# Kernel optimization log

Measured on AMD Instinct MI355X. Metric: run time of the kernel, lower is better.

## Reference

```python
import jax, jax.numpy as jnp
import numpy as np

B, C, S, K, HEADS, P = 2, 64, 112, 7, 4, 3
DH = C // HEADS

def _na_idx(L, k):
    # NATTEN-style clamped windows: each query attends to k in-bounds neighbors
    i = np.arange(L)
    s = np.clip(i - k // 2, 0, L - k)
    nbr = s[:, None] + np.arange(k)[None, :]      # (L,k) absolute neighbor index
    rel = nbr - i[:, None] + (k - 1)              # (L,k) rel-pos-bias index in [0,2k-2]
    return jnp.asarray(nbr), jnp.asarray(rel)

def _ln(x, g, b, eps=1e-5):
    m = jnp.mean(x, -1, keepdims=True)
    v = jnp.mean(jnp.square(x - m), -1, keepdims=True)
    return (x - m) * jax.lax.rsqrt(v + eps) * g + b

def _conv(x, w, b):
    y = jax.lax.conv_general_dilated(x, w, (1, 1), [(P // 2, P // 2)] * 2,
                                     dimension_numbers=('NCHW', 'OIHW', 'NCHW'))
    return jnp.transpose(y + b[None, :, None, None], (0, 2, 3, 1))  # NHWC

def setup_inputs():
    key = jax.random.key(0)
    ks = jax.random.split(key, 24)
    r = lambda i, shape, s=0.02: jax.random.normal(ks[i], shape, jnp.float32) * s
    return {
        'xq': jax.random.normal(ks[0], (B, C, S, S), jnp.float32),
        'xkv': jax.random.normal(ks[1], (B, C, S, S), jnp.float32),
        'conv_w_s': r(2, (C, C, P, P)), 'conv_b_s': r(3, (C,), 0.01),
        'conv_w_l': r(4, (C, C, P, P)), 'conv_b_l': r(5, (C,), 0.01),
        'g_s': jnp.ones((C,), jnp.float32), 'b_s': jnp.zeros((C,), jnp.float32),
        'g_l': jnp.ones((C,), jnp.float32), 'b_l': jnp.zeros((C,), jnp.float32),
        'Wq': r(6, (C, C)), 'bq': r(7, (C,), 0.01),
        'Wk': r(8, (C, C)), 'bk': r(9, (C,), 0.01),
        'Wv': r(10, (C, C)), 'bv': r(11, (C,), 0.01),
        'Wo': r(12, (C, C)), 'bo': r(13, (C,), 0.01),
        'rpb': r(14, (HEADS, 2 * K - 1, 2 * K - 1)),
        'g_n': jnp.ones((C,), jnp.float32), 'b_n': jnp.zeros((C,), jnp.float32),
        'W1': r(15, (C, 2 * C)), 'b1': r(16, (2 * C,), 0.01),
        'W2': r(17, (2 * C, C)), 'b2': r(18, (C,), 0.01),
    }

def reference(xq, xkv, conv_w_s, conv_b_s, conv_w_l, conv_b_l, g_s, b_s, g_l, b_l,
              Wq, bq, Wk, bk, Wv, bv, Wo, bo, rpb, g_n, b_n, W1, b1, W2, b2):
    emb_q = _conv(xq, conv_w_s, conv_b_s)     # (B,H,W,C) overlap patch embed (q branch)
    emb_kv = _conv(xkv, conv_w_l, conv_b_l)   # (B,H,W,C)
    Hh, Ww = emb_q.shape[1], emb_q.shape[2]
    qn = _ln(emb_q, g_s, b_s)
    kvn = _ln(emb_kv, g_l, b_l)
    q = (qn @ Wq + bq).reshape(B, Hh, Ww, HEADS, DH)
    k = (kvn @ Wk + bk).reshape(B, Hh, Ww, HEADS, DH)
    v = (kvn @ Wv + bv).reshape(B, Hh, Ww, HEADS, DH)
    ni, ri = _na_idx(Hh, K)
    nj, rj = _na_idx(Ww, K)

    def gather(t):  # (B,H,W,h,d) -> (B,H,W,K*K,h,d) neighborhood windows
        t = t[:, ni]                                 # (B,H,K,W,h,d)
        t = t[:, :, :, nj]                           # (B,H,K,W,K,h,d)
        t = jnp.transpose(t, (0, 1, 3, 2, 4, 5, 6))  # (B,H,W,K,K,h,d)
        return t.reshape(B, Hh, Ww, K * K, HEADS, DH)

    kg, vg = gather(k), gather(v)
    logits = jnp.einsum('bijhd,bijnhd->bhijn', q, kg) * (DH ** -0.5)
    bias = rpb[:, ri]                                # (h,H,K,2K-1)
    bias = bias[:, :, :, rj]                         # (h,H,K,W,K)
    bias = jnp.transpose(bias, (0, 1, 3, 2, 4)).reshape(HEADS, Hh, Ww, K * K)
    attn = jax.nn.softmax(logits + bias[None], axis=-1)
    out = jnp.einsum('bhijn,bijnhd->bijhd', attn, vg).reshape(B, Hh, Ww, C)
    att = out @ Wo + bo + emb_kv                     # residual with kv embedding
    x = _ln(att, g_n, b_n)
    x = jax.nn.gelu(x @ W1 + b1, approximate=False) @ W2 + b2 + att
    return jnp.transpose(x, (0, 3, 1, 2))            # (B,C,H,W)
```

## Files before the change

### kernel.cpp

```cpp
#include <hip/hip_runtime.h>
#include <math.h>

#define SS 112
#define HW (SS*SS)
#define NPIX (2*HW)

typedef __bf16 v8bf __attribute__((ext_vector_type(8)));
typedef short  v8s  __attribute__((ext_vector_type(8)));
typedef float  v4f  __attribute__((ext_vector_type(4)));

__device__ __forceinline__ unsigned short f2bf(float f){
  unsigned u = __builtin_bit_cast(unsigned, f);
  u = (u + 0x7fffu + ((u >> 16) & 1u)) >> 16;
  return (unsigned short)u;
}
__device__ __forceinline__ unsigned cvt_pk_bf16(float lo, float hi){
  unsigned r;
  asm("v_cvt_pk_bf16_f32 %0, %1, %2" : "=v"(r) : "v"(lo), "v"(hi));
  return r;
}
__device__ __forceinline__ v8bf zero8(){
  v8s z = {0,0,0,0,0,0,0,0};
  return __builtin_bit_cast(v8bf, z);
}
__device__ __forceinline__ float gelu_fast(float x){
  float u = fmaf(0.044715f*x, x, 1.0f);
  float z = fminf(2.3021178f * x * u, 80.0f);
  float s = exp2f(z);
  return x * s * __builtin_amdgcn_rcpf(s + 1.0f);
}

struct Params {
  const float *xq, *xkv, *cws, *cwl, *Wq, *Wk, *Wv, *Wo, *W1, *W2, *rpb;
  const float *cbs, *g_s, *b_s, *cbl, *g_l, *b_l;
  const float *bq, *bk, *bv, *bo, *gn, *bn, *b1, *b2;
  unsigned short *WBs, *WBl, *WBq, *WBk, *WBv, *WBo, *WB1, *WB2;
  float *rpb2g;
  unsigned short *xTq, *xTkv, *qb, *kb, *vT;
  float *emb, *outp;
};

__device__ __forceinline__ void pack_wconv(const float* __restrict__ w,
                                           unsigned short* __restrict__ WB, int idx){
  int lane = idx & 63, tslot = (idx >> 6) & 3, kk = idx >> 8;
  int tap = kk >> 1;
  int ic0 = ((kk & 1) << 5) + ((lane >> 4) << 3);
  int oc  = tslot*16 + (lane & 15);
  union { unsigned short u[8]; uint4 q; } pk;
  #pragma unroll
  for (int i = 0; i < 8; ++i) pk.u[i] = f2bf(w[(oc*64 + ic0 + i)*9 + tap]);
  ((uint4*)WB)[idx] = pk.q;
}
__device__ __forceinline__ void pack_wlin(const float* __restrict__ W,
                                          unsigned short* __restrict__ WB,
                                          int N, int idx){
  int lane = idx & 63;
  int tmp = idx >> 6;
  int tiles = N >> 4;
  int tslot = tmp % tiles;
  int kk = tmp / tiles;
  int k0 = kk*32 + ((lane >> 4) << 3);
  int oc = tslot*16 + (lane & 15);
  union { unsigned short u[8]; uint4 q; } pk;
  #pragma unroll
  for (int i = 0; i < 8; ++i) pk.u[i] = f2bf(W[(size_t)(k0 + i)*N + oc]);
  ((uint4*)WB)[idx] = pk.q;
}

__global__ __launch_bounds__(256) void k_prep_s(Params P)
{
  __shared__ float tile[64][68];
  const int u = blockIdx.x, tid = threadIdx.x;
  if (u >= 784){
    const int pu = u - 784;
    if      (pu < 18) pack_wconv(P.cws, P.WBs, pu*256 + tid);
    else if (pu < 36) pack_wconv(P.cwl, P.WBl, (pu-18)*256 + tid);
    else if (pu < 38) pack_wlin(P.Wq, P.WBq, 64,  (pu-36)*256 + tid);
    else if (pu < 40) pack_wlin(P.Wk, P.WBk, 64,  (pu-38)*256 + tid);
    else if (pu < 42) pack_wlin(P.Wv, P.WBv, 64,  (pu-40)*256 + tid);
    else if (pu < 44) pack_wlin(P.Wo, P.WBo, 64,  (pu-42)*256 + tid);
    else if (pu < 48) pack_wlin(P.W1, P.WB1, 128, (pu-44)*256 + tid);
    else if (pu < 52) pack_wlin(P.W2, P.WB2, 64,  (pu-48)*256 + tid);
    else {
      int idx = (pu-52)*256 + tid;
      if (idx < 4*169) P.rpb2g[idx] = P.rpb[idx] * 1.4426950408889634f;
    }
    return;
  }
  const int inst = u >= 392 ? 1 : 0;
  const float* x = inst ? P.xkv : P.xq;
  unsigned short* xT = inst ? P.xTkv : P.xTq;
  const int base = (u - inst*392) * 64;
  const int b = base / HW;
  const int r0 = base - b*HW;
  {
    const int cc = tid >> 2, xo = (tid & 3) << 4;
    const float* src = x + ((size_t)(b*64 + cc))*HW + r0 + xo;
    float4 v0 = ((const float4*)src)[0];
    float4 v1 = ((const float4*)src)[1];
    float4 v2 = ((const float4*)src)[2];
    float4 v3 = ((const float4*)src)[3];
    float* dst = &tile[cc][xo];
    ((float4*)dst)[0] = v0; ((float4*)dst)[1] = v1;
    ((float4*)dst)[2] = v2; ((float4*)dst)[3] = v3;
  }
  __syncthreads();
  {
    const int px = tid >> 2, co = (tid & 3) << 4;
    union { unsigned short uu[16]; uint4 q[2]; } pk;
    #pragma unroll
    for (int i = 0; i < 16; ++i) pk.uu[i] = f2bf(tile[co + i][px]);
    uint4* dst = (uint4*)(xT + ((size_t)(base + px))*64 + co);
    dst[0] = pk.q[0]; dst[1] = pk.q[1];
  }
}

__global__ __launch_bounds__(256) void k_conv_s(Params P)
{
  __shared__ unsigned short nlds4[4][1024];
  const int tid = threadIdx.x;
  const int wid = tid >> 6, l = tid & 63;
  const int g = l >> 4, c = l & 15;
  unsigned short* nlds = nlds4[wid];
  const int u = blockIdx.x;
  const int inst = u >= 392 ? 1 : 0;
  const int P0 = ((u - inst*392)*4 + wid) * 16;

  const unsigned short* xT  = inst ? P.xTkv : P.xTq;
  const unsigned short* WBc = inst ? P.WBl : P.WBs;
  const float* cb    = inst ? P.cbl : P.cbs;
  const float* gamma = inst ? P.g_l : P.g_s;
  const float* beta  = inst ? P.b_l : P.b_s;

  const int p = P0 + c;
  const int b = p / HW, r = p - b*HW;
  const int py = r / SS, pxx = r - py*SS;
  const int pb64 = b*HW;

  float cbv[4], gv[4], bev[4];
  #pragma unroll
  for (int t = 0; t < 4; ++t){
    cbv[t] = cb[c + 16*t]; gv[t] = gamma[c + 16*t]; bev[t] = beta[c + 16*t];
  }

  v4f acc[4];
  #pragma unroll
  for (int t = 0; t < 4; ++t) acc[t] = (v4f){cbv[t], cbv[t], cbv[t], cbv[t]};

  const int icg = g << 3;
  #pragma unroll
  for (int kk = 0; kk < 18; ++kk){
    const int tap = kk >> 1;
    const int dy = tap/3 - 1, dx = tap - (tap/3)*3 - 1;
    const int icof = ((kk & 1) << 5) + icg;
    int yy = py + dy, xx = pxx + dx;
    bool ok = ((unsigned)yy < SS) && ((unsigned)xx < SS);
    v8bf a = zero8();
    if (ok) a = *(const v8bf*)(xT + ((size_t)(pb64 + yy*SS + xx))*64 + icof);
    #pragma unroll
    for (int t = 0; t < 4; ++t){
      v8bf bfr = *(const v8bf*)(WBc + ((size_t)((kk*4 + t)*64 + l))*8);
      acc[t] = __builtin_amdgcn_mfma_f32_16x16x32_bf16(a, bfr, acc[t], 0, 0, 0);
    }
  }

  if (inst){
    #pragma unroll
    for (int t = 0; t < 4; ++t)
      #pragma unroll
      for (int r2 = 0; r2 < 4; ++r2)
        P.emb[((size_t)(P0 + 4*g + r2))*64 + c + 16*t] = acc[t][r2];
  }

  {
    float mean[4], inv[4];
    #pragma unroll
    for (int r2 = 0; r2 < 4; ++r2){
      float s = acc[0][r2] + acc[1][r2] + acc[2][r2] + acc[3][r2];
      s += __shfl_xor(s, 1, 64); s += __shfl_xor(s, 2, 64);
      s += __shfl_xor(s, 4, 64); s += __shfl_xor(s, 8, 64);
      mean[r2] = s * (1.f/64.f);
      float d0 = acc[0][r2] - mean[r2], d1 = acc[1][r2] - mean[r2];
      float d2 = acc[2][r2] - mean[r2], d3 = acc[3][r2] - mean[r2];
      float vs = d0*d0 + d1*d1 + d2*d2 + d3*d3;
      vs += __shfl_xor(vs, 1, 64); vs += __shfl_xor(vs, 2, 64);
      vs += __shfl_xor(vs, 4, 64); vs += __shfl_xor(vs, 8, 64);
      inv[r2] = rsqrtf(vs * (1.f/64.f) + 1e-5f);
    }
    #pragma unroll
    for (int t = 0; t < 4; ++t){
      int c16 = 2*t + (c >> 3);
      #pragma unroll
      for (int r2 = 0; r2 < 4; r2 += 2){
        int row0 = 4*g + r2, row1 = row0 + 1;
        float n0 = (acc[t][r2]   - mean[r2])   * inv[r2]   * gv[t] + bev[t];
        float n1 = (acc[t][r2+1] - mean[r2+1]) * inv[r2+1] * gv[t] + bev[t];
        unsigned w = cvt_pk_bf16(n0, n1);
        nlds[row0*64 + (((c16 ^ (row0 & 7)) << 3) | (c & 7))] = (unsigned short)(w & 0xffffu);
        nlds[row1*64 + (((c16 ^ (row1 & 7)) << 3) | (c & 7))] = (unsigned short)(w >> 16);
      }
    }
  }

  #pragma unroll
  for (int which = 0; which < 2; ++which){
    if (which == 1 && !inst) break;
    const unsigned short* WB = which ? P.WBv : (inst ? P.WBk : P.WBq);
    const float* bias        = which ? P.bv : (inst ? P.bk : P.bq);

    float pb[4];
    #pragma unroll
    for (int t = 0; t < 4; ++t) pb[t] = bias[c + 16*t];
    v4f pa[4];
    #pragma unroll
    for (int t = 0; t < 4; ++t) pa[t] = (v4f){pb[t], pb[t], pb[t], pb[t]};

    #pragma unroll
    for (int kk = 0; kk < 2; ++kk){
      v8bf av = *(const v8bf*)(nlds + c*64 + (((kk*4 + g) ^ (c & 7)) << 3));
      #pragma unroll
      for (int t = 0; t < 4; ++t){
        v8bf bfr = *(const v8bf*)(WB + ((size_t)((kk*4 + t)*64 + l))*8);
        pa[t] = __builtin_amdgcn_mfma_f32_16x16x32_bf16(av, bfr, pa[t], 0, 0, 0);
      }
    }
    if (which == 0){
      unsigned short* outp = inst ? P.kb : P.qb;
      #pragma unroll
      for (int t = 0; t < 4; ++t)
        #pragma unroll
        for (int r2 = 0; r2 < 4; r2 += 2){
          unsigned w = cvt_pk_bf16(pa[t][r2], pa[t][r2+1]);
          outp[((size_t)(P0 + 4*g + r2))*64 + c + 16*t]   = (unsigned short)(w & 0xffffu);
          outp[((size_t)(P0 + 4*g + r2+1))*64 + c + 16*t] = (unsigned short)(w >> 16);
        }
    } else {
      #pragma unroll
      for (int t = 0; t < 4; ++t){
        uint2 w2;
        w2.x = cvt_pk_bf16(pa[t][0], pa[t][1]);
        w2.y = cvt_pk_bf16(pa[t][2], pa[t][3]);
        *(uint2*)(P.vT + (size_t)(c + 16*t)*NPIX + (P0 + 4*g)) = w2;
      }
    }
  }
}

__global__ __launch_bounds__(256) void k_nattenout(Params P)
{
  __shared__ __align__(16) unsigned short alds[64*72];
  __shared__ __align__(16) unsigned char smem[24576];
  const int tid = threadIdx.x;
  const int wid = tid >> 6, l = tid & 63;
  const int g = l >> 4, c = l & 15;
  const int blk = blockIdx.x;

  for (int s = 0; s < 4; ++s){
    const int u = blk*4 + s;
    const int h = wid;
    const int p0 = u * 16;
    const int b = p0 / HW, r0 = p0 - b*HW;
    const int i = r0 / SS, j0 = r0 - i*SS;

    const int si = min(max(i - 3, 0), SS - 7);
    const int aj = (min(max(j0 - 3, 0), SS - 22)) & ~7;
    const int oi = si - i + 6;
    const int pbase = b*HW;

    const int j   = j0 + c;
    const int sjp = min(max(j - 3, 0), SS - 7);
    const int adj = 8*g + (aj - sjp);
    const float* bp = P.rpb2g + h*169 + oi*13 + (8*g + aj - j + 6);

    v8bf bq = zero8();
    if (g < 2) bq = *(const v8bf*)(P.qb + (size_t)(p0 + c)*64 + h*16 + 8*g);

    float lt[14][4];
    const int arow = 8*(c >> 2) + (c & 3);
    #pragma unroll
    for (int tau = 0; tau < 14; ++tau){
      const int t = tau >> 1;
      int kpix = pbase + (si + t)*SS + aj + arow + 4*(tau & 1);
      kpix = min(kpix, NPIX - 1);
      v8bf ak = zero8();
      if (g < 2) ak = *(const v8bf*)(P.kb + (size_t)kpix*64 + h*16 + 8*g);
      v4f a0 = {0.f,0.f,0.f,0.f};
      a0 = __builtin_amdgcn_mfma_f32_16x16x32_bf16(ak, bq, a0, 0, 0, 0);
      lt[tau][0]=a0[0]; lt[tau][1]=a0[1]; lt[tau][2]=a0[2]; lt[tau][3]=a0[3];
    }

    const float SC = 0.3606737602222409f;
    float mx4[4] = {-3e38f,-3e38f,-3e38f,-3e38f};
    #pragma unroll
    for (int tau = 0; tau < 14; ++tau){
      const int t = tau >> 1;
      #pragma unroll
      for (int r = 0; r < 4; ++r){
        const int cc = 4*(tau & 1) + r;
        float bias = bp[t*13 + cc];
        float lg = fmaf(lt[tau][r], SC, bias);
        lt[tau][r] = ((unsigned)(adj + cc) <= 6u) ? lg : -1e30f;
        mx4[r] = fmaxf(mx4[r], lt[tau][r]);
      }
    }
    float mx = fmaxf(fmaxf(mx4[0], mx4[1]), fmaxf(mx4[2], mx4[3]));
    mx = fmaxf(mx, __shfl_xor(mx, 16, 64));
    mx = fmaxf(mx, __shfl_xor(mx, 32, 64));
    float es4[4] = {0.f,0.f,0.f,0.f};
    #pragma unroll
    for (int tau = 0; tau < 14; ++tau)
      #pragma unroll
      for (int r = 0; r < 4; ++r){
        float pexp = exp2f(lt[tau][r] - mx);
        lt[tau][r] = pexp;
        es4[r] += pexp;
      }
    float es = (es4[0] + es4[1]) + (es4[2] + es4[3]);
    es += __shfl_xor(es, 16, 64);
    es += __shfl_xor(es, 32, 64);
    const float inv = 1.0f / es;

    const unsigned short* vrow = P.vT + (size_t)(h*16 + c)*NPIX;
    v4f oacc = {0.f,0.f,0.f,0.f};
    #pragma unroll
    for (int t = 0; t < 7; ++t){
      union { unsigned w[4]; v8bf bf; } pa;
      pa.w[0] = cvt_pk_bf16(lt[2*t][0]*inv,   lt[2*t][1]*inv);
      pa.w[1] = cvt_pk_bf16(lt[2*t][2]*inv,   lt[2*t][3]*inv);
      pa.w[2] = cvt_pk_bf16(lt[2*t+1][0]*inv, lt[2*t+1][1]*inv);
      pa.w[3] = cvt_pk_bf16(lt[2*t+1][2]*inv, lt[2*t+1][3]*inv);
      int vpixb = pbase + (si + t)*SS + aj + 8*g;
      vpixb = min(vpixb, NPIX - 8);
      v8bf bv = *(const v8bf*)(vrow + vpixb);
      oacc = __builtin_amdgcn_mfma_f32_16x16x32_bf16(pa.bf, bv, oacc, 0, 0, 0);
    }

    #pragma unroll
    for (int r = 0; r < 4; r += 2){
      unsigned w = cvt_pk_bf16(oacc[r], oacc[r+1]);
      alds[(s*16 + 4*g + r)*72   + h*16 + c] = (unsigned short)(w & 0xffffu);
      alds[(s*16 + 4*g + r+1)*72 + h*16 + c] = (unsigned short)(w >> 16);
    }
  }
  __syncthreads();

  {
    unsigned short* ylds = (unsigned short*)smem + wid*1024;
    unsigned short* hlds = (unsigned short*)(smem + 8192) + wid*2048;
    const int P0 = blk*64 + wid*16;
    const int b = P0 / HW;
    const int ijb = P0 - b*HW;

    v4f att[4];
    #pragma unroll
    for (int t = 0; t < 4; ++t){
      float bb = P.bo[c + 16*t];
      #pragma unroll
      for (int r = 0; r < 4; ++r)
        att[t][r] = bb + P.emb[((size_t)(P0 + 4*g + r))*64 + c + 16*t];
    }
    #pragma unroll
    for (int kk = 0; kk < 2; ++kk){
      v8bf a = *(const v8bf*)(alds + (wid*16 + c)*72 + kk*32 + 8*g);
      #pragma unroll
      for (int t = 0; t < 4; ++t){
        v8bf bfr = *(const v8bf*)(P.WBo + ((size_t)((kk*4 + t)*64 + l))*8);
        att[t] = __builtin_amdgcn_mfma_f32_16x16x32_bf16(a, bfr, att[t], 0, 0, 0);
      }
    }

    {
      float gv[4], bev[4];
      #pragma unroll
      for (int t = 0; t < 4; ++t){ gv[t] = P.gn[c + 16*t]; bev[t] = P.bn[c + 16*t]; }
      float mean[4], inv[4];
      #pragma unroll
      for (int r = 0; r < 4; ++r){
        float s = att[0][r] + att[1][r] + att[2][r] + att[3][r];
        s += __shfl_xor(s, 1, 64); s += __shfl_xor(s, 2, 64);
        s += __shfl_xor(s, 4, 64); s += __shfl_xor(s, 8, 64);
        mean[r] = s * (1.f/64.f);
        float d0 = att[0][r] - mean[r], d1 = att[1][r] - mean[r];
        float d2 = att[2][r] - mean[r], d3 = att[3][r] - mean[r];
        float vs = d0*d0 + d1*d1 + d2*d2 + d3*d3;
        vs += __shfl_xor(vs, 1, 64); vs += __shfl_xor(vs, 2, 64);
        vs += __shfl_xor(vs, 4, 64); vs += __shfl_xor(vs, 8, 64);
        inv[r] = rsqrtf(vs * (1.f/64.f) + 1e-5f);
      }
      #pragma unroll
      for (int t = 0; t < 4; ++t){
        int c16 = 2*t + (c >> 3);
        #pragma unroll
        for (int r = 0; r < 4; r += 2){
          int row0 = 4*g + r, row1 = row0 + 1;
          float n0 = (att[t][r]   - mean[r])   * inv[r]   * gv[t] + bev[t];
          float n1 = (att[t][r+1] - mean[r+1]) * inv[r+1] * gv[t] + bev[t];
          unsigned w = cvt_pk_bf16(n0, n1);
          ylds[row0*64 + (((c16 ^ (row0 & 7)) << 3) | (c & 7))] = (unsigned short)(w & 0xffffu);
          ylds[row1*64 + (((c16 ^ (row1 & 7)) << 3) | (c & 7))] = (unsigned short)(w >> 16);
        }
      }
    }

    v4f hc[8];
    #pragma unroll
    for (int tt = 0; tt < 8; ++tt){
      float bb = P.b1[c + 16*tt];
      hc[tt] = (v4f){bb,bb,bb,bb};
    }
    #pragma unroll
    for (int kk = 0; kk < 2; ++kk){
      v8bf a = *(const v8bf*)(ylds + c*64 + (((kk*4 + g) ^ (c & 7)) << 3));
      #pragma unroll
      for (int tt = 0; tt < 8; ++tt){
        v8bf bfr = *(const v8bf*)(P.WB1 + ((size_t)((kk*8 + tt)*64 + l))*8);
        hc[tt] = __builtin_amdgcn_mfma_f32_16x16x32_bf16(a, bfr, hc[tt], 0, 0, 0);
      }
    }
    #pragma unroll
    for (int tt = 0; tt < 8; ++tt){
      int chunk = 2*tt + (c >> 3);
      #pragma unroll
      for (int r = 0; r < 4; r += 2){
        int row0 = 4*g + r, row1 = row0 + 1;
        int swz0 = (chunk & 8) | ((chunk & 7) ^ (row0 & 7));
        int swz1 = (chunk & 8) | ((chunk & 7) ^ (row1 & 7));
        unsigned w = cvt_pk_bf16(gelu_fast(hc[tt][r]), gelu_fast(hc[tt][r+1]));
        hlds[row0*128 + swz0*8 + (c & 7)] = (unsigned short)(w & 0xffffu);
        hlds[row1*128 + swz1*8 + (c & 7)] = (unsigned short)(w >> 16);
      }
    }

    v4f xc[4];
    #pragma unroll
    for (int t = 0; t < 4; ++t){
      float bb = P.b2[c + 16*t];
      #pragma unroll
      for (int r = 0; r < 4; ++r)
        xc[t][r] = bb + att[t][r];
    }
    #pragma unroll
    for (int kk = 0; kk < 4; ++kk){
      int chunk = 4*kk + g;
      int swz = (chunk & 8) | ((chunk & 7) ^ (c & 7));
      v8bf a = *(const v8bf*)(hlds + c*128 + swz*8);
      #pragma unroll
      for (int t = 0; t < 4; ++t){
        v8bf bfr = *(const v8bf*)(P.WB2 + ((size_t)((kk*4 + t)*64 + l))*8);
        xc[t] = __builtin_amdgcn_mfma_f32_16x16x32_bf16(a, bfr, xc[t], 0, 0, 0);
      }
    }
    #pragma unroll
    for (int t = 0; t < 4; ++t)
      #pragma unroll
      for (int r = 0; r < 4; ++r)
        P.outp[((size_t)(b*64 + c + 16*t))*HW + ijb + 4*g + r] = xc[t][r];
  }
}

extern "C" void kernel_launch(void* const* d_in, const int* in_sizes, int n_in,
                              void* d_out, int out_size, void* d_ws, size_t ws_size,
                              hipStream_t stream) {
  Params P;
  P.xq  = (const float*)d_in[0];
  P.xkv = (const float*)d_in[1];
  P.cws = (const float*)d_in[2];
  P.cbs = (const float*)d_in[3];
  P.cwl = (const float*)d_in[4];
  P.cbl = (const float*)d_in[5];
  P.g_s = (const float*)d_in[6];
  P.b_s = (const float*)d_in[7];
  P.g_l = (const float*)d_in[8];
  P.b_l = (const float*)d_in[9];
  P.Wq  = (const float*)d_in[10];
  P.bq  = (const float*)d_in[11];
  P.Wk  = (const float*)d_in[12];
  P.bk  = (const float*)d_in[13];
  P.Wv  = (const float*)d_in[14];
  P.bv  = (const float*)d_in[15];
  P.Wo  = (const float*)d_in[16];
  P.bo  = (const float*)d_in[17];
  P.rpb = (const float*)d_in[18];
  P.gn  = (const float*)d_in[19];
  P.bn  = (const float*)d_in[20];
  P.W1  = (const float*)d_in[21];
  P.b1  = (const float*)d_in[22];
  P.W2  = (const float*)d_in[23];
  P.b2  = (const float*)d_in[24];

  unsigned short* xTq  = (unsigned short*)d_ws;
  unsigned short* xTkv = xTq  + (size_t)NPIX*64;
  unsigned short* WBs  = xTkv + (size_t)NPIX*64;
  unsigned short* WBl  = WBs  + 36864;
  unsigned short* WBq  = WBl  + 36864;
  unsigned short* WBk  = WBq  + 4096;
  unsigned short* WBv  = WBk  + 4096;
  unsigned short* WBo  = WBv  + 4096;
  unsigned short* WB1  = WBo  + 4096;
  unsigned short* WB2  = WB1  + 8192;
  unsigned short* qb   = WB2  + 8192;
  unsigned short* kb   = qb   + (size_t)NPIX*64;
  unsigned short* vT   = kb   + (size_t)NPIX*64;
  float* emb   = (float*)(vT + (size_t)NPIX*64);
  float* rpb2a = emb + (size_t)NPIX*64;
  float* rpb2g = rpb2a + 64;

  P.WBs = WBs; P.WBl = WBl; P.WBq = WBq; P.WBk = WBk; P.WBv = WBv;
  P.WBo = WBo; P.WB1 = WB1; P.WB2 = WB2;
  P.rpb2g = rpb2g;
  P.xTq = xTq; P.xTkv = xTkv; P.qb = qb; P.kb = kb; P.vT = vT;
  P.emb = emb; P.outp = (float*)d_out;

  hipLaunchKernelGGL(k_prep_s,    dim3(839), dim3(256), 0, stream, P);
  hipLaunchKernelGGL(k_conv_s,    dim3(784), dim3(256), 0, stream, P);
  hipLaunchKernelGGL(k_nattenout, dim3(392), dim3(256), 0, stream, P);
}
```

Before: 82.80 us.

## Split fused attention+MLP kernel into separate natten and output kernels, remap blocks

The fused attention/output kernel, which looped over 4 sub-tiles per block before an LDS barrier, is split into a neighborhood-attention kernel with 1568 blocks and an output-projection/MLP kernel with 392 blocks. The two kernels communicate through a new bf16 global buffer. Conv and attention block indices are also swizzled across 8 groups, likely to spread work across XCDs and L2 caches. The split adds parallelism and removes the serial sub-tile loop, at the cost of an extra launch and a global round-trip for the attention output.

Result: faster. 70.70 us, median of 2 (-14.6%).

```diff
diff --git a/kernel.cpp b/kernel.cpp
--- a/kernel.cpp
+++ b/kernel.cpp
@@ -36,7 +36,7 @@
   const float *bq, *bk, *bv, *bo, *gn, *bn, *b1, *b2;
   unsigned short *WBs, *WBl, *WBq, *WBk, *WBv, *WBo, *WB1, *WB2;
   float *rpb2g;
-  unsigned short *xTq, *xTkv, *qb, *kb, *vT;
+  unsigned short *xTq, *xTkv, *qb, *kb, *vT, *aob;
   float *emb, *outp;
 };
 
@@ -122,7 +122,7 @@
   const int wid = tid >> 6, l = tid & 63;
   const int g = l >> 4, c = l & 15;
   unsigned short* nlds = nlds4[wid];
-  const int u = blockIdx.x;
+  const int u = (blockIdx.x & 7)*98 + (blockIdx.x >> 3);
   const int inst = u >= 392 ? 1 : 0;
   const int P0 = ((u - inst*392)*4 + wid) * 16;
 
@@ -246,216 +246,213 @@
   }
 }
 
-__global__ __launch_bounds__(256) void k_nattenout(Params P)
+__global__ __launch_bounds__(256) void k_natten_s(Params P)
 {
-  __shared__ __align__(16) unsigned short alds[64*72];
+  const int l = threadIdx.x & 63;
+  const int h = threadIdx.x >> 6;
+  const int u = (blockIdx.x & 7)*196 + (blockIdx.x >> 3);
+  const int c = l & 15, g = l >> 4;
+  const int p0 = u * 16;
+  const int b = p0 / HW, r0 = p0 - b*HW;
+  const int i = r0 / SS, j0 = r0 - i*SS;
+
+  const int si = min(max(i - 3, 0), SS - 7);
+  const int aj = (min(max(j0 - 3, 0), SS - 22)) & ~7;
+  const int oi = si - i + 6;
+  const int pbase = b*HW;
+
+  const int j   = j0 + c;
+  const int sjp = min(max(j - 3, 0), SS - 7);
+  const int adj = 8*g + (aj - sjp);
+  const float* bp = P.rpb2g + h*169 + oi*13 + (8*g + aj - j + 6);
+
+  v8bf bq = zero8();
+  if (g < 2) bq = *(const v8bf*)(P.qb + (size_t)(p0 + c)*64 + h*16 + 8*g);
+
+  float lt[14][4];
+  const int arow = 8*(c >> 2) + (c & 3);
+  #pragma unroll
+  for (int tau = 0; tau < 14; ++tau){
+    const int t = tau >> 1;
+    int kpix = pbase + (si + t)*SS + aj + arow + 4*(tau & 1);
+    kpix = min(kpix, NPIX - 1);
+    v8bf ak = zero8();
+    if (g < 2) ak = *(const v8bf*)(P.kb + (size_t)kpix*64 + h*16 + 8*g);
+    v4f a0 = {0.f,0.f,0.f,0.f};
+    a0 = __builtin_amdgcn_mfma_f32_16x16x32_bf16(ak, bq, a0, 0, 0, 0);
+    lt[tau][0]=a0[0]; lt[tau][1]=a0[1]; lt[tau][2]=a0[2]; lt[tau][3]=a0[3];
+  }
+
+  const float SC = 0.3606737602222409f;
+  float mx4[4] = {-3e38f,-3e38f,-3e38f,-3e38f};
+  #pragma unroll
+  for (int tau = 0; tau < 14; ++tau){
+    const int t = tau >> 1;
+    #pragma unroll
+    for (int r = 0; r < 4; ++r){
+      const int cc = 4*(tau & 1) + r;
+      float bias = bp[t*13 + cc];
+      float lg = fmaf(lt[tau][r], SC, bias);
+      lt[tau][r] = ((unsigned)(adj + cc) <= 6u) ? lg : -1e30f;
+      mx4[r] = fmaxf(mx4[r], lt[tau][r]);
+    }
+  }
+  float mx = fmaxf(fmaxf(mx4[0], mx4[1]), fmaxf(mx4[2], mx4[3]));
+  mx = fmaxf(mx, __shfl_xor(mx, 16, 64));
+  mx = fmaxf(mx, __shfl_xor(mx, 32, 64));
+  float es4[4] = {0.f,0.f,0.f,0.f};
+  #pragma unroll
+  for (int tau = 0; tau < 14; ++tau)
+    #pragma unroll
+    for (int r = 0; r < 4; ++r){
+      float pexp = exp2f(lt[tau][r] - mx);
+      lt[tau][r] = pexp;
+      es4[r] += pexp;
+    }
+  float es = (es4[0] + es4[1]) + (es4[2] + es4[3]);
+  es += __shfl_xor(es, 16, 64);
+  es += __shfl_xor(es, 32, 64);
+  const float inv = 1.0f / es;
+
+  const unsigned short* vrow = P.vT + (size_t)(h*16 + c)*NPIX;
+  v4f oacc = {0.f,0.f,0.f,0.f};
+  #pragma unroll
+  for (int t = 0; t < 7; ++t){
+    union { unsigned w[4]; v8bf bf; } pa;
+    pa.w[0] = cvt_pk_bf16(lt[2*t][0]*inv,   lt[2*t][1]*inv);
+    pa.w[1] = cvt_pk_bf16(lt[2*t][2]*inv,   lt[2*t][3]*inv);
+    pa.w[2] = cvt_pk_bf16(lt[2*t+1][0]*inv, lt[2*t+1][1]*inv);
+    pa.w[3] = cvt_pk_bf16(lt[2*t+1][2]*inv, lt[2*t+1][3]*inv);
+    int vpixb = pbase + (si + t)*SS + aj + 8*g;
+    vpixb = min(vpixb, NPIX - 8);
+    v8bf bv = *(const v8bf*)(vrow + vpixb);
+    oacc = __builtin_amdgcn_mfma_f32_16x16x32_bf16(pa.bf, bv, oacc, 0, 0, 0);
+  }
+
+  #pragma unroll
+  for (int r = 0; r < 4; r += 2){
+    unsigned w = cvt_pk_bf16(oacc[r], oacc[r+1]);
+    P.aob[(size_t)(p0 + 4*g + r)*64 + h*16 + c]   = (unsigned short)(w & 0xffffu);
+    P.aob[(size_t)(p0 + 4*g + r+1)*64 + h*16 + c] = (unsigned short)(w >> 16);
+  }
+}
+
+__global__ __launch_bounds__(256) void k_out_s(Params P)
+{
   __shared__ __align__(16) unsigned char smem[24576];
   const int tid = threadIdx.x;
   const int wid = tid >> 6, l = tid & 63;
   const int g = l >> 4, c = l & 15;
-  const int blk = blockIdx.x;
-
-  for (int s = 0; s < 4; ++s){
-    const int u = blk*4 + s;
-    const int h = wid;
-    const int p0 = u * 16;
-    const int b = p0 / HW, r0 = p0 - b*HW;
-    const int i = r0 / SS, j0 = r0 - i*SS;
-
-    const int si = min(max(i - 3, 0), SS - 7);
-    const int aj = (min(max(j0 - 3, 0), SS - 22)) & ~7;
-    const int oi = si - i + 6;
-    const int pbase = b*HW;
-
-    const int j   = j0 + c;
-    const int sjp = min(max(j - 3, 0), SS - 7);
-    const int adj = 8*g + (aj - sjp);
-    const float* bp = P.rpb2g + h*169 + oi*13 + (8*g + aj - j + 6);
-
-    v8bf bq = zero8();
-    if (g < 2) bq = *(const v8bf*)(P.qb + (size_t)(p0 + c)*64 + h*16 + 8*g);
-
-    float lt[14][4];
-    const int arow = 8*(c >> 2) + (c & 3);
-    #pragma unroll
-    for (int tau = 0; tau < 14; ++tau){
-      const int t = tau >> 1;
-      int kpix = pbase + (si + t)*SS + aj + arow + 4*(tau & 1);
-      kpix = min(kpix, NPIX - 1);
-      v8bf ak = zero8();
-      if (g < 2) ak = *(const v8bf*)(P.kb + (size_t)kpix*64 + h*16 + 8*g);
-      v4f a0 = {0.f,0.f,0.f,0.f};
-      a0 = __builtin_amdgcn_mfma_f32_16x16x32_bf16(ak, bq, a0, 0, 0, 0);
-      lt[tau][0]=a0[0]; lt[tau][1]=a0[1]; lt[tau][2]=a0[2]; lt[tau][3]=a0[3];
-    }
-
-    const float SC = 0.3606737602222409f;
-    float mx4[4] = {-3e38f,-3e38f,-3e38f,-3e38f};
-    #pragma unroll
-    for (int tau = 0; tau < 14; ++tau){
-      const int t = tau >> 1;
-      #pragma unroll
-      for (int r = 0; r < 4; ++r){
-        const int cc = 4*(tau & 1) + r;
-        float bias = bp[t*13 + cc];
-        float lg = fmaf(lt[tau][r], SC, bias);
-        lt[tau][r] = ((unsigned)(adj + cc) <= 6u) ? lg : -1e30f;
-        mx4[r] = fmaxf(mx4[r], lt[tau][r]);
-      }
-    }
-    float mx = fmaxf(fmaxf(mx4[0], mx4[1]), fmaxf(mx4[2], mx4[3]));
-    mx = fmaxf(mx, __shfl_xor(mx, 16, 64));
-    mx = fmaxf(mx, __shfl_xor(mx, 32, 64));
-    float es4[4] = {0.f,0.f,0.f,0.f};
-    #pragma unroll
-    for (int tau = 0; tau < 14; ++tau)
-      #pragma unroll
-      for (int r = 0; r < 4; ++r){
-        float pexp = exp2f(lt[tau][r] - mx);
-        lt[tau][r] = pexp;
-        es4[r] += pexp;
-      }
-    float es = (es4[0] + es4[1]) + (es4[2] + es4[3]);
-    es += __shfl_xor(es, 16, 64);
-    es += __shfl_xor(es, 32, 64);
-    const float inv = 1.0f / es;
-
-    const unsigned short* vrow = P.vT + (size_t)(h*16 + c)*NPIX;
-    v4f oacc = {0.f,0.f,0.f,0.f};
-    #pragma unroll
-    for (int t = 0; t < 7; ++t){
-      union { unsigned w[4]; v8bf bf; } pa;
-      pa.w[0] = cvt_pk_bf16(lt[2*t][0]*inv,   lt[2*t][1]*inv);
-      pa.w[1] = cvt_pk_bf16(lt[2*t][2]*inv,   lt[2*t][3]*inv);
-      pa.w[2] = cvt_pk_bf16(lt[2*t+1][0]*inv, lt[2*t+1][1]*inv);
-      pa.w[3] = cvt_pk_bf16(lt[2*t+1][2]*inv, lt[2*t+1][3]*inv);
-      int vpixb = pbase + (si + t)*SS + aj + 8*g;
-      vpixb = min(vpixb, NPIX - 8);
-      v8bf bv = *(const v8bf*)(vrow + vpixb);
-      oacc = __builtin_amdgcn_mfma_f32_16x16x32_bf16(pa.bf, bv, oacc, 0, 0, 0);
-    }
-
-    #pragma unroll
-    for (int r = 0; r < 4; r += 2){
-      unsigned w = cvt_pk_bf16(oacc[r], oacc[r+1]);
-      alds[(s*16 + 4*g + r)*72   + h*16 + c] = (unsigned short)(w & 0xffffu);
-      alds[(s*16 + 4*g + r+1)*72 + h*16 + c] = (unsigned short)(w >> 16);
-    }
-  }
-  __syncthreads();
+  unsigned short* ylds = (unsigned short*)smem + wid*1024;
+  unsigned short* hlds = (unsigned short*)(smem + 8192) + wid*2048;
+  const int P0 = (blockIdx.x*4 + wid) * 16;
+  const int b = P0 / HW;
+  const int ijb = P0 - b*HW;
+
+  v4f att[4];
+  #pragma unroll
+  for (int t = 0; t < 4; ++t){
+    float bb = P.bo[c + 16*t];
+    #pragma unroll
+    for (int r = 0; r < 4; ++r)
+      att[t][r] = bb + P.emb[((size_t)(P0 + 4*g + r))*64 + c + 16*t];
+  }
+  #pragma unroll
+  for (int kk = 0; kk < 2; ++kk){
+    v8bf a = *(const v8bf*)(P.aob + (size_t)(P0 + c)*64 + kk*32 + 8*g);
+    #pragma unroll
+    for (int t = 0; t < 4; ++t){
+      v8bf bfr = *(const v8bf*)(P.WBo + ((size_t)((kk*4 + t)*64 + l))*8);
+      att[t] = __builtin_amdgcn_mfma_f32_16x16x32_bf16(a, bfr, att[t], 0, 0, 0);
+    }
+  }
 
   {
-    unsigned short* ylds = (unsigned short*)smem + wid*1024;
-    unsigned short* hlds = (unsigned short*)(smem + 8192) + wid*2048;
-    const int P0 = blk*64 + wid*16;
-    const int b = P0 / HW;
-    const int ijb = P0 - b*HW;
-
-    v4f att[4];
+    float gv[4], bev[4];
+    #pragma unroll
+    for (int t = 0; t < 4; ++t){ gv[t] = P.gn[c + 16*t]; bev[t] = P.bn[c + 16*t]; }
+    float mean[4], inv[4];
+    #pragma unroll
+    for (int r = 0; r < 4; ++r){
+      float s = att[0][r] + att[1][r] + att[2][r] + att[3][r];
+      s += __shfl_xor(s, 1, 64); s += __shfl_xor(s, 2, 64);
+      s += __shfl_xor(s, 4, 64); s += __shfl_xor(s, 8, 64);
+      mean[r] = s * (1.f/64.f);
+      float d0 = att[0][r] - mean[r], d1 = att[1][r] - mean[r];
+      float d2 = att[2][r] - mean[r], d3 = att[3][r] - mean[r];
+      float vs = d0*d0 + d1*d1 + d2*d2 + d3*d3;
+      vs += __shfl_xor(vs, 1, 64); vs += __shfl_xor(vs, 2, 64);
+      vs += __shfl_xor(vs, 4, 64); vs += __shfl_xor(vs, 8, 64);
+      inv[r] = rsqrtf(vs * (1.f/64.f) + 1e-5f);
+    }
     #pragma unroll
     for (int t = 0; t < 4; ++t){
-      float bb = P.bo[c + 16*t];
-      #pragma unroll
-      for (int r = 0; r < 4; ++r)
-        att[t][r] = bb + P.emb[((size_t)(P0 + 4*g + r))*64 + c + 16*t];
-    }
-    #pragma unroll
-    for (int kk = 0; kk < 2; ++kk){
-      v8bf a = *(const v8bf*)(alds + (wid*16 + c)*72 + kk*32 + 8*g);
-      #pragma unroll
-      for (int t = 0; t < 4; ++t){
-        v8bf bfr = *(const v8bf*)(P.WBo + ((size_t)((kk*4 + t)*64 + l))*8);
-        att[t] = __builtin_amdgcn_mfma_f32_16x16x32_bf16(a, bfr, att[t], 0, 0, 0);
-      }
-    }
-
-    {
-      float gv[4], bev[4];
-      #pragma unroll
-      for (int t = 0; t < 4; ++t){ gv[t] = P.gn[c + 16*t]; bev[t] = P.bn[c + 16*t]; }
-      float mean[4], inv[4];
-      #pragma unroll
-      for (int r = 0; r < 4; ++r){
-        float s = att[0][r] + att[1][r] + att[2][r] + att[3][r];
-        s += __shfl_xor(s, 1, 64); s += __shfl_xor(s, 2, 64);
-        s += __shfl_xor(s, 4, 64); s += __shfl_xor(s, 8, 64);
-        mean[r] = s * (1.f/64.f);
-        float d0 = att[0][r] - mean[r], d1 = att[1][r] - mean[r];
-        float d2 = att[2][r] - mean[r], d3 = att[3][r] - mean[r];
-        float vs = d0*d0 + d1*d1 + d2*d2 + d3*d3;
-        vs += __shfl_xor(vs, 1, 64); vs += __shfl_xor(vs, 2, 64);
-        vs += __shfl_xor(vs, 4, 64); vs += __shfl_xor(vs, 8, 64);
-        inv[r] = rsqrtf(vs * (1.f/64.f) + 1e-5f);
-      }
-      #pragma unroll
-      for (int t = 0; t < 4; ++t){
-        int c16 = 2*t + (c >> 3);
-        #pragma unroll
-        for (int r = 0; r < 4; r += 2){
-          int row0 = 4*g + r, row1 = row0 + 1;
-          float n0 = (att[t][r]   - mean[r])   * inv[r]   * gv[t] + bev[t];
-          float n1 = (att[t][r+1] - mean[r+1]) * inv[r+1] * gv[t] + bev[t];
-          unsigned w = cvt_pk_bf16(n0, n1);
-          ylds[row0*64 + (((c16 ^ (row0 & 7)) << 3) | (c & 7))] = (unsigned short)(w & 0xffffu);
-          ylds[row1*64 + (((c16 ^ (row1 & 7)) << 3) | (c & 7))] = (unsigned short)(w >> 16);
-        }
-      }
-    }
-
-    v4f hc[8];
-    #pragma unroll
-    for (int tt = 0; tt < 8; ++tt){
-      float bb = P.b1[c + 16*tt];
-      hc[tt] = (v4f){bb,bb,bb,bb};
-    }
-    #pragma unroll
-    for (int kk = 0; kk < 2; ++kk){
-      v8bf a = *(const v8bf*)(ylds + c*64 + (((kk*4 + g) ^ (c & 7)) << 3));
-      #pragma unroll
-      for (int tt = 0; tt < 8; ++tt){
-        v8bf bfr = *(const v8bf*)(P.WB1 + ((size_t)((kk*8 + tt)*64 + l))*8);
-        hc[tt] = __builtin_amdgcn_mfma_f32_16x16x32_bf16(a, bfr, hc[tt], 0, 0, 0);
-      }
-    }
-    #pragma unroll
-    for (int tt = 0; tt < 8; ++tt){
-      int chunk = 2*tt + (c >> 3);
+      int c16 = 2*t + (c >> 3);
       #pragma unroll
       for (int r = 0; r < 4; r += 2){
         int row0 = 4*g + r, row1 = row0 + 1;
-        int swz0 = (chunk & 8) | ((chunk & 7) ^ (row0 & 7));
-        int swz1 = (chunk & 8) | ((chunk & 7) ^ (row1 & 7));
-        unsigned w = cvt_pk_bf16(gelu_fast(hc[tt][r]), gelu_fast(hc[tt][r+1]));
-        hlds[row0*128 + swz0*8 + (c & 7)] = (unsigned short)(w & 0xffffu);
-        hlds[row1*128 + swz1*8 + (c & 7)] = (unsigned short)(w >> 16);
+        float n0 = (att[t][r]   - mean[r])   * inv[r]   * gv[t] + bev[t];
+        float n1 = (att[t][r+1] - mean[r+1]) * inv[r+1] * gv[t] + bev[t];
+        unsigned w = cvt_pk_bf16(n0, n1);
+        ylds[row0*64 + (((c16 ^ (row0 & 7)) << 3) | (c & 7))] = (unsigned short)(w & 0xffffu);
+        ylds[row1*64 + (((c16 ^ (row1 & 7)) << 3) | (c & 7))] = (unsigned short)(w >> 16);
       }
     }
-
-    v4f xc[4];
+  }
+
+  v4f hc[8];
+  #pragma unroll
+  for (int tt = 0; tt < 8; ++tt){
+    float bb = P.b1[c + 16*tt];
+    hc[tt] = (v4f){bb,bb,bb,bb};
+  }
+  #pragma unroll
+  for (int kk = 0; kk < 2; ++kk){
+    v8bf a = *(const v8bf*)(ylds + c*64 + (((kk*4 + g) ^ (c & 7)) << 3));
+    #pragma unroll
+    for (int tt = 0; tt < 8; ++tt){
+      v8bf bfr = *(const v8bf*)(P.WB1 + ((size_t)((kk*8 + tt)*64 + l))*8);
+      hc[tt] = __builtin_amdgcn_mfma_f32_16x16x32_bf16(a, bfr, hc[tt], 0, 0, 0);
+    }
+  }
+  #pragma unroll
+  for (int tt = 0; tt < 8; ++tt){
+    int chunk = 2*tt + (c >> 3);
+    #pragma unroll
+    for (int r = 0; r < 4; r += 2){
+      int row0 = 4*g + r, row1 = row0 + 1;
+      int swz0 = (chunk & 8) | ((chunk & 7) ^ (row0 & 7));
+      int swz1 = (chunk & 8) | ((chunk & 7) ^ (row1 & 7));
+      unsigned w = cvt_pk_bf16(gelu_fast(hc[tt][r]), gelu_fast(hc[tt][r+1]));
+      hlds[row0*128 + swz0*8 + (c & 7)] = (unsigned short)(w & 0xffffu);
+      hlds[row1*128 + swz1*8 + (c & 7)] = (unsigned short)(w >> 16);
+    }
+  }
+
+  v4f xc[4];
+  #pragma unroll
+  for (int t = 0; t < 4; ++t){
+    float bb = P.b2[c + 16*t];
+    #pragma unroll
+    for (int r = 0; r < 4; ++r)
+      xc[t][r] = bb + att[t][r];
+  }
+  #pragma unroll
+  for (int kk = 0; kk < 4; ++kk){
+    int chunk = 4*kk + g;
+    int swz = (chunk & 8) | ((chunk & 7) ^ (c & 7));
+    v8bf a = *(const v8bf*)(hlds + c*128 + swz*8);
     #pragma unroll
     for (int t = 0; t < 4; ++t){
-      float bb = P.b2[c + 16*t];
-      #pragma unroll
-      for (int r = 0; r < 4; ++r)
-        xc[t][r] = bb + att[t][r];
-    }
-    #pragma unroll
-    for (int kk = 0; kk < 4; ++kk){
-      int chunk = 4*kk + g;
-      int swz = (chunk & 8) | ((chunk & 7) ^ (c & 7));
-      v8bf a = *(const v8bf*)(hlds + c*128 + swz*8);
-      #pragma unroll
-      for (int t = 0; t < 4; ++t){
-        v8bf bfr = *(const v8bf*)(P.WB2 + ((size_t)((kk*4 + t)*64 + l))*8);
-        xc[t] = __builtin_amdgcn_mfma_f32_16x16x32_bf16(a, bfr, xc[t], 0, 0, 0);
-      }
-    }
-    #pragma unroll
-    for (int t = 0; t < 4; ++t)
-      #pragma unroll
-      for (int r = 0; r < 4; ++r)
-        P.outp[((size_t)(b*64 + c + 16*t))*HW + ijb + 4*g + r] = xc[t][r];
-  }
+      v8bf bfr = *(const v8bf*)(P.WB2 + ((size_t)((kk*4 + t)*64 + l))*8);
+      xc[t] = __builtin_amdgcn_mfma_f32_16x16x32_bf16(a, bfr, xc[t], 0, 0, 0);
+    }
+  }
+  #pragma unroll
+  for (int t = 0; t < 4; ++t)
+    #pragma unroll
+    for (int r = 0; r < 4; ++r)
+      P.outp[((size_t)(b*64 + c + 16*t))*HW + ijb + 4*g + r] = xc[t][r];
 }
 
 extern "C" void kernel_launch(void* const* d_in, const int* in_sizes, int n_in,
@@ -501,17 +498,19 @@
   unsigned short* qb   = WB2  + 8192;
   unsigned short* kb   = qb   + (size_t)NPIX*64;
   unsigned short* vT   = kb   + (size_t)NPIX*64;
-  float* emb   = (float*)(vT + (size_t)NPIX*64);
+  unsigned short* aob  = vT   + (size_t)NPIX*64;
+  float* emb   = (float*)(aob + (size_t)NPIX*64);
   float* rpb2a = emb + (size_t)NPIX*64;
   float* rpb2g = rpb2a + 64;
 
   P.WBs = WBs; P.WBl = WBl; P.WBq = WBq; P.WBk = WBk; P.WBv = WBv;
   P.WBo = WBo; P.WB1 = WB1; P.WB2 = WB2;
   P.rpb2g = rpb2g;
-  P.xTq = xTq; P.xTkv = xTkv; P.qb = qb; P.kb = kb; P.vT = vT;
+  P.xTq = xTq; P.xTkv = xTkv; P.qb = qb; P.kb = kb; P.vT = vT; P.aob = aob;
   P.emb = emb; P.outp = (float*)d_out;
 
-  hipLaunchKernelGGL(k_prep_s,    dim3(839), dim3(256), 0, stream, P);
-  hipLaunchKernelGGL(k_conv_s,    dim3(784), dim3(256), 0, stream, P);
-  hipLaunchKernelGGL(k_nattenout, dim3(392), dim3(256), 0, stream, P);
-}
+  hipLaunchKernelGGL(k_prep_s,   dim3(839),  dim3(256), 0, stream, P);
+  hipLaunchKernelGGL(k_conv_s,   dim3(784),  dim3(256), 0, stream, P);
+  hipLaunchKernelGGL(k_natten_s, dim3(1568), dim3(256), 0, stream, P);
+  hipLaunchKernelGGL(k_out_s,    dim3(392),  dim3(256), 0, stream, P);
+}
```

## Split fused natten+MLP kernel into 16-pixel blocks with cross-wave LayerNorm

Applied to the files above, without the earlier changes.

The fused attention/output-projection/MLP kernel no longer has each block loop over four 16-pixel groups. Each block now handles one 16-pixel group, launching four times as many blocks, and the four waves split the output channels of every GEMM. LayerNorm statistics are reduced across waves through shared memory using sum and sum-of-squares, which adds extra barriers and a small numerical risk from the E[x^2]-m^2 variance form. Block indices in both the conv and attention kernels are remapped with a stride permutation to spread neighbouring tiles across CUs/XCDs, and the final output store becomes a float4 write.

Measured after the change: 69.37 us. 1.19x faster.

```diff
diff --git a/kernel.cpp b/kernel.cpp
--- a/kernel.cpp
+++ b/kernel.cpp
@@ -122,7 +122,7 @@
   const int wid = tid >> 6, l = tid & 63;
   const int g = l >> 4, c = l & 15;
   unsigned short* nlds = nlds4[wid];
-  const int u = blockIdx.x;
+  const int u = (blockIdx.x & 7)*98 + (blockIdx.x >> 3);
   const int inst = u >= 392 ? 1 : 0;
   const int P0 = ((u - inst*392)*4 + wid) * 16;
 
@@ -246,22 +246,23 @@
   }
 }
 
-__global__ __launch_bounds__(256) void k_nattenout(Params P)
+__global__ __launch_bounds__(256) void k_natten_out(Params P)
 {
-  __shared__ __align__(16) unsigned short alds[64*72];
-  __shared__ __align__(16) unsigned char smem[24576];
+  __shared__ __align__(16) unsigned short alds[16*72];
+  __shared__ __align__(16) unsigned short ylds[16*64];
+  __shared__ __align__(16) unsigned short hlds[16*128];
+  __shared__ float part_s[4][16];
+  __shared__ float part_q[4][16];
   const int tid = threadIdx.x;
   const int wid = tid >> 6, l = tid & 63;
-  const int g = l >> 4, c = l & 15;
-  const int blk = blockIdx.x;
-
-  for (int s = 0; s < 4; ++s){
-    const int u = blk*4 + s;
-    const int h = wid;
-    const int p0 = u * 16;
-    const int b = p0 / HW, r0 = p0 - b*HW;
-    const int i = r0 / SS, j0 = r0 - i*SS;
-
+  const int h = wid;
+  const int c = l & 15, g = l >> 4;
+  const int u = (blockIdx.x & 7)*196 + (blockIdx.x >> 3);
+  const int p0 = u * 16;
+  const int b = p0 / HW, r0 = p0 - b*HW;
+  const int i = r0 / SS, j0 = r0 - i*SS;
+
+  {
     const int si = min(max(i - 3, 0), SS - 7);
     const int aj = (min(max(j0 - 3, 0), SS - 22)) & ~7;
     const int oi = si - i + 6;
@@ -338,123 +339,122 @@
     #pragma unroll
     for (int r = 0; r < 4; r += 2){
       unsigned w = cvt_pk_bf16(oacc[r], oacc[r+1]);
-      alds[(s*16 + 4*g + r)*72   + h*16 + c] = (unsigned short)(w & 0xffffu);
-      alds[(s*16 + 4*g + r+1)*72 + h*16 + c] = (unsigned short)(w >> 16);
+      alds[(4*g + r)*72   + h*16 + c] = (unsigned short)(w & 0xffffu);
+      alds[(4*g + r+1)*72 + h*16 + c] = (unsigned short)(w >> 16);
     }
   }
   __syncthreads();
 
-  {
-    unsigned short* ylds = (unsigned short*)smem + wid*1024;
-    unsigned short* hlds = (unsigned short*)(smem + 8192) + wid*2048;
-    const int P0 = blk*64 + wid*16;
-    const int b = P0 / HW;
-    const int ijb = P0 - b*HW;
-
-    v4f att[4];
-    #pragma unroll
-    for (int t = 0; t < 4; ++t){
-      float bb = P.bo[c + 16*t];
-      #pragma unroll
-      for (int r = 0; r < 4; ++r)
-        att[t][r] = bb + P.emb[((size_t)(P0 + 4*g + r))*64 + c + 16*t];
-    }
+  const int ijb = p0 - b*HW;
+  const int cw = c + 16*wid;
+
+  v4f att;
+  {
+    float bb = P.bo[cw];
+    #pragma unroll
+    for (int r = 0; r < 4; ++r)
+      att[r] = bb + P.emb[((size_t)(p0 + 4*g + r))*64 + cw];
     #pragma unroll
     for (int kk = 0; kk < 2; ++kk){
-      v8bf a = *(const v8bf*)(alds + (wid*16 + c)*72 + kk*32 + 8*g);
-      #pragma unroll
-      for (int t = 0; t < 4; ++t){
-        v8bf bfr = *(const v8bf*)(P.WBo + ((size_t)((kk*4 + t)*64 + l))*8);
-        att[t] = __builtin_amdgcn_mfma_f32_16x16x32_bf16(a, bfr, att[t], 0, 0, 0);
-      }
-    }
-
-    {
-      float gv[4], bev[4];
-      #pragma unroll
-      for (int t = 0; t < 4; ++t){ gv[t] = P.gn[c + 16*t]; bev[t] = P.bn[c + 16*t]; }
-      float mean[4], inv[4];
+      v8bf a = *(const v8bf*)(alds + c*72 + kk*32 + 8*g);
+      v8bf bfr = *(const v8bf*)(P.WBo + ((size_t)((kk*4 + wid)*64 + l))*8);
+      att = __builtin_amdgcn_mfma_f32_16x16x32_bf16(a, bfr, att, 0, 0, 0);
+    }
+  }
+
+  {
+    float s4[4], q4[4];
+    #pragma unroll
+    for (int r = 0; r < 4; ++r){
+      float s = att[r], q = att[r]*att[r];
+      s += __shfl_xor(s, 1, 64); q += __shfl_xor(q, 1, 64);
+      s += __shfl_xor(s, 2, 64); q += __shfl_xor(q, 2, 64);
+      s += __shfl_xor(s, 4, 64); q += __shfl_xor(q, 4, 64);
+      s += __shfl_xor(s, 8, 64); q += __shfl_xor(q, 8, 64);
+      s4[r] = s; q4[r] = q;
+    }
+    if (c == 0){
       #pragma unroll
       for (int r = 0; r < 4; ++r){
-        float s = att[0][r] + att[1][r] + att[2][r] + att[3][r];
-        s += __shfl_xor(s, 1, 64); s += __shfl_xor(s, 2, 64);
-        s += __shfl_xor(s, 4, 64); s += __shfl_xor(s, 8, 64);
-        mean[r] = s * (1.f/64.f);
-        float d0 = att[0][r] - mean[r], d1 = att[1][r] - mean[r];
-        float d2 = att[2][r] - mean[r], d3 = att[3][r] - mean[r];
-        float vs = d0*d0 + d1*d1 + d2*d2 + d3*d3;
-        vs += __shfl_xor(vs, 1, 64); vs += __shfl_xor(vs, 2, 64);
-        vs += __shfl_xor(vs, 4, 64); vs += __shfl_xor(vs, 8, 64);
-        inv[r] = rsqrtf(vs * (1.f/64.f) + 1e-5f);
-      }
-      #pragma unroll
-      for (int t = 0; t < 4; ++t){
-        int c16 = 2*t + (c >> 3);
-        #pragma unroll
-        for (int r = 0; r < 4; r += 2){
-          int row0 = 4*g + r, row1 = row0 + 1;
-          float n0 = (att[t][r]   - mean[r])   * inv[r]   * gv[t] + bev[t];
-          float n1 = (att[t][r+1] - mean[r+1]) * inv[r+1] * gv[t] + bev[t];
-          unsigned w = cvt_pk_bf16(n0, n1);
-          ylds[row0*64 + (((c16 ^ (row0 & 7)) << 3) | (c & 7))] = (unsigned short)(w & 0xffffu);
-          ylds[row1*64 + (((c16 ^ (row1 & 7)) << 3) | (c & 7))] = (unsigned short)(w >> 16);
-        }
-      }
-    }
-
-    v4f hc[8];
-    #pragma unroll
-    for (int tt = 0; tt < 8; ++tt){
+        part_s[wid][4*g + r] = s4[r];
+        part_q[wid][4*g + r] = q4[r];
+      }
+    }
+  }
+  __syncthreads();
+  {
+    float gv = P.gn[cw], bev = P.bn[cw];
+    const int c16 = 2*wid + (c >> 3);
+    #pragma unroll
+    for (int r = 0; r < 4; r += 2){
+      int row0 = 4*g + r, row1 = row0 + 1;
+      float ts0 = part_s[0][row0] + part_s[1][row0] + part_s[2][row0] + part_s[3][row0];
+      float tq0 = part_q[0][row0] + part_q[1][row0] + part_q[2][row0] + part_q[3][row0];
+      float ts1 = part_s[0][row1] + part_s[1][row1] + part_s[2][row1] + part_s[3][row1];
+      float tq1 = part_q[0][row1] + part_q[1][row1] + part_q[2][row1] + part_q[3][row1];
+      float m0 = ts0 * (1.f/64.f), m1 = ts1 * (1.f/64.f);
+      float v0 = tq0 * (1.f/64.f) - m0*m0;
+      float v1 = tq1 * (1.f/64.f) - m1*m1;
+      float i0 = rsqrtf(v0 + 1e-5f), i1 = rsqrtf(v1 + 1e-5f);
+      float n0 = (att[r]   - m0) * i0 * gv + bev;
+      float n1 = (att[r+1] - m1) * i1 * gv + bev;
+      unsigned w = cvt_pk_bf16(n0, n1);
+      ylds[row0*64 + (((c16 ^ (row0 & 7)) << 3) | (c & 7))] = (unsigned short)(w & 0xffffu);
+      ylds[row1*64 + (((c16 ^ (row1 & 7)) << 3) | (c & 7))] = (unsigned short)(w >> 16);
+    }
+  }
+  __syncthreads();
+
+  {
+    v4f hc[2];
+    #pragma unroll
+    for (int q = 0; q < 2; ++q){
+      int tt = 2*wid + q;
       float bb = P.b1[c + 16*tt];
-      hc[tt] = (v4f){bb,bb,bb,bb};
+      hc[q] = (v4f){bb,bb,bb,bb};
     }
     #pragma unroll
     for (int kk = 0; kk < 2; ++kk){
       v8bf a = *(const v8bf*)(ylds + c*64 + (((kk*4 + g) ^ (c & 7)) << 3));
       #pragma unroll
-      for (int tt = 0; tt < 8; ++tt){
+      for (int q = 0; q < 2; ++q){
+        int tt = 2*wid + q;
         v8bf bfr = *(const v8bf*)(P.WB1 + ((size_t)((kk*8 + tt)*64 + l))*8);
-        hc[tt] = __builtin_amdgcn_mfma_f32_16x16x32_bf16(a, bfr, hc[tt], 0, 0, 0);
-      }
-    }
-    #pragma unroll
-    for (int tt = 0; tt < 8; ++tt){
+        hc[q] = __builtin_amdgcn_mfma_f32_16x16x32_bf16(a, bfr, hc[q], 0, 0, 0);
+      }
+    }
+    #pragma unroll
+    for (int q = 0; q < 2; ++q){
+      int tt = 2*wid + q;
       int chunk = 2*tt + (c >> 3);
       #pragma unroll
       for (int r = 0; r < 4; r += 2){
         int row0 = 4*g + r, row1 = row0 + 1;
         int swz0 = (chunk & 8) | ((chunk & 7) ^ (row0 & 7));
         int swz1 = (chunk & 8) | ((chunk & 7) ^ (row1 & 7));
-        unsigned w = cvt_pk_bf16(gelu_fast(hc[tt][r]), gelu_fast(hc[tt][r+1]));
+        unsigned w = cvt_pk_bf16(gelu_fast(hc[q][r]), gelu_fast(hc[q][r+1]));
         hlds[row0*128 + swz0*8 + (c & 7)] = (unsigned short)(w & 0xffffu);
         hlds[row1*128 + swz1*8 + (c & 7)] = (unsigned short)(w >> 16);
       }
     }
-
-    v4f xc[4];
-    #pragma unroll
-    for (int t = 0; t < 4; ++t){
-      float bb = P.b2[c + 16*t];
-      #pragma unroll
-      for (int r = 0; r < 4; ++r)
-        xc[t][r] = bb + att[t][r];
-    }
+  }
+  __syncthreads();
+
+  {
+    v4f xc;
+    float bb = P.b2[cw];
+    #pragma unroll
+    for (int r = 0; r < 4; ++r) xc[r] = bb + att[r];
     #pragma unroll
     for (int kk = 0; kk < 4; ++kk){
       int chunk = 4*kk + g;
       int swz = (chunk & 8) | ((chunk & 7) ^ (c & 7));
       v8bf a = *(const v8bf*)(hlds + c*128 + swz*8);
-      #pragma unroll
-      for (int t = 0; t < 4; ++t){
-        v8bf bfr = *(const v8bf*)(P.WB2 + ((size_t)((kk*4 + t)*64 + l))*8);
-        xc[t] = __builtin_amdgcn_mfma_f32_16x16x32_bf16(a, bfr, xc[t], 0, 0, 0);
-      }
-    }
-    #pragma unroll
-    for (int t = 0; t < 4; ++t)
-      #pragma unroll
-      for (int r = 0; r < 4; ++r)
-        P.outp[((size_t)(b*64 + c + 16*t))*HW + ijb + 4*g + r] = xc[t][r];
+      v8bf bfr = *(const v8bf*)(P.WB2 + ((size_t)((kk*4 + wid)*64 + l))*8);
+      xc = __builtin_amdgcn_mfma_f32_16x16x32_bf16(a, bfr, xc, 0, 0, 0);
+    }
+    *(float4*)(P.outp + ((size_t)(b*64 + cw))*HW + ijb + 4*g) =
+        __builtin_bit_cast(float4, xc);
   }
 }
 
@@ -511,7 +511,7 @@
   P.xTq = xTq; P.xTkv = xTkv; P.qb = qb; P.kb = kb; P.vT = vT;
   P.emb = emb; P.outp = (float*)d_out;
 
-  hipLaunchKernelGGL(k_prep_s,    dim3(839), dim3(256), 0, stream, P);
-  hipLaunchKernelGGL(k_conv_s,    dim3(784), dim3(256), 0, stream, P);
-  hipLaunchKernelGGL(k_nattenout, dim3(392), dim3(256), 0, stream, P);
-}
+  hipLaunchKernelGGL(k_prep_s,     dim3(839),  dim3(256), 0, stream, P);
+  hipLaunchKernelGGL(k_conv_s,     dim3(784),  dim3(256), 0, stream, P);
+  hipLaunchKernelGGL(k_natten_out, dim3(1568), dim3(256), 0, stream, P);
+}
```
